# Kernel optimization log

Measured on AMD Instinct MI355X. Metric: run time of the kernel, lower is better.

Reference implementation:

```python
import jax, jax.numpy as jnp
import numpy as np

B, H, T, D = 4, 16, 4096, 128

def setup_inputs() -> dict:
    key = jax.random.key(0)
    kq, kk, kv = jax.random.split(key, 3)
    Q = jax.random.normal(kq, (B, H, T, D), dtype=jnp.float32)
    K = jax.random.normal(kk, (B, H, T, D), dtype=jnp.float32)
    V = jax.random.normal(kv, (B, H, T, D), dtype=jnp.float32)
    return {"Q": Q, "K": K, "V": V}

def reference(Q, K, V):
    # Unnormalized linear attention: Q @ K^T @ V.
    # Algebraically reassociated as Q @ (K^T @ V) to avoid the [T, T] intermediate:
    # kv: [B,H,D,D]
    kv = jnp.einsum('bhtd,bhte->bhde', K, V)
    return jnp.einsum('bhtd,bhde->bhte', Q, kv)
```

## Files before the change

### kernel.cpp

```cpp
#include <hip/hip_runtime.h>
#include <stdint.h>

typedef __attribute__((ext_vector_type(8))) short short8;
typedef __attribute__((ext_vector_type(4))) float floatx4;

#define T_DIM 4096
#define D_DIM 128
#define BH_TOT 64
#define NCHUNK 8
#define CHUNK (T_DIM / NCHUNK)
#define LSTRIDE 72

__device__ __forceinline__ unsigned short f2bf(float f) {
  unsigned int u = __float_as_uint(f);
  u = (u + 0x7FFFu + ((u >> 16) & 1u)) >> 16;
  return (unsigned short)u;
}

__device__ __forceinline__ unsigned int pack2(float lo, float hi) {
  return (unsigned int)f2bf(lo) | ((unsigned int)f2bf(hi) << 16);
}

__global__ __launch_bounds__(256, 2)
void kv_phase1(const float* __restrict__ K, const float* __restrict__ V,
               float* __restrict__ kvT) {
  const int bh    = blockIdx.y;
  const int chunk = blockIdx.x;
  const int tid   = threadIdx.x;
  const int lane  = tid & 63;
  const int wv    = tid >> 6;
  const int c     = tid & 31;
  const int r     = tid >> 5;
  const int m0    = (wv >> 1) * 64;
  const int n0    = (wv & 1) * 64;

  __shared__ unsigned short Vt[128 * LSTRIDE];
  __shared__ unsigned short Kt[128 * LSTRIDE];

  floatx4 acc[4][4];
#pragma unroll
  for (int i = 0; i < 4; ++i)
#pragma unroll
    for (int j = 0; j < 4; ++j) acc[i][j] = (floatx4){0.f, 0.f, 0.f, 0.f};

  const size_t base = ((size_t)bh * T_DIM + (size_t)chunk * CHUNK) * D_DIM;
  const float* Vp = V + base + 4 * c;
  const float* Kp = K + base + 4 * c;

  float4 ld[2][8];
  uint4  pk[2][4];

  auto load_tile = [&](int tile) {
    const size_t roff = (size_t)(tile * 64 + 8 * r) * D_DIM;
#pragma unroll
    for (int i = 0; i < 8; ++i) {
      ld[0][i] = *(const float4*)(Vp + roff + (size_t)i * D_DIM);
      ld[1][i] = *(const float4*)(Kp + roff + (size_t)i * D_DIM);
    }
  };

  auto pack_all = [&]() {
#pragma unroll
    for (int op = 0; op < 2; ++op)
#pragma unroll
      for (int j = 0; j < 4; ++j) {
        uint4 v;
        v.x = (unsigned int)f2bf(((const float*)&ld[op][0])[j]) |
              ((unsigned int)f2bf(((const float*)&ld[op][1])[j]) << 16);
        v.y = (unsigned int)f2bf(((const float*)&ld[op][2])[j]) |
              ((unsigned int)f2bf(((const float*)&ld[op][3])[j]) << 16);
        v.z = (unsigned int)f2bf(((const float*)&ld[op][4])[j]) |
              ((unsigned int)f2bf(((const float*)&ld[op][5])[j]) << 16);
        v.w = (unsigned int)f2bf(((const float*)&ld[op][6])[j]) |
              ((unsigned int)f2bf(((const float*)&ld[op][7])[j]) << 16);
        pk[op][j] = v;
      }
  };

  load_tile(0);
  pack_all();

  for (int tile = 0; tile < CHUNK / 64; ++tile) {
    if (tile < CHUNK / 64 - 1) load_tile(tile + 1);
    __syncthreads();
#pragma unroll
    for (int j = 0; j < 4; ++j) {
      *(uint4*)&Vt[(4 * c + j) * LSTRIDE + 8 * r] = pk[0][j];
      *(uint4*)&Kt[(4 * c + j) * LSTRIDE + 8 * r] = pk[1][j];
    }
    __syncthreads();

#pragma unroll
    for (int ks = 0; ks < 2; ++ks) {
      const int koff = 32 * ks + 8 * (lane >> 4);
      short8 af[4], bf[4];
#pragma unroll
      for (int tm = 0; tm < 4; ++tm)
        af[tm] = *(const short8*)&Vt[(m0 + tm * 16 + (lane & 15)) * LSTRIDE + koff];
#pragma unroll
      for (int tn = 0; tn < 4; ++tn)
        bf[tn] = *(const short8*)&Kt[(n0 + tn * 16 + (lane & 15)) * LSTRIDE + koff];
#pragma unroll
      for (int tm = 0; tm < 4; ++tm)
#pragma unroll
        for (int tn = 0; tn < 4; ++tn)
          acc[tm][tn] = __builtin_amdgcn_mfma_f32_16x16x32_bf16(af[tm], bf[tn],
                                                                acc[tm][tn], 0, 0, 0);
    }
    if (tile < CHUNK / 64 - 1) pack_all();
  }

  float* dst = kvT + (size_t)bh * (128 * 128);
  const int col = lane & 15;
  const int rb  = (lane >> 4) * 4;
#pragma unroll
  for (int tm = 0; tm < 4; ++tm)
#pragma unroll
    for (int tn = 0; tn < 4; ++tn)
#pragma unroll
      for (int rg = 0; rg < 4; ++rg) {
        const int e = m0 + tm * 16 + rb + rg;
        const int d = n0 + tn * 16 + col;
        unsafeAtomicAdd(&dst[e * 128 + d], acc[tm][tn][rg]);
      }
}

__global__ __launch_bounds__(256, 2)
void qkv_phase2(const float* __restrict__ Q, const float* __restrict__ kvT,
                float* __restrict__ out) {
  const int bh   = blockIdx.y;
  const int t0   = blockIdx.x * 128;
  const int tid  = threadIdx.x;
  const int lane = tid & 63;
  const int wv   = tid >> 6;
  const int c    = tid & 15;
  const int rq   = tid >> 4;
  const int m0   = (wv >> 1) * 64;
  const int n0   = (wv & 1) * 64;

  __shared__ unsigned short Qs[128 * LSTRIDE];
  __shared__ unsigned short Bs[128 * LSTRIDE];

  const float* Qp = Q + ((size_t)bh * T_DIM + t0) * D_DIM;
  const float* Bp = kvT + (size_t)bh * (128 * 128);

  floatx4 acc[4][4];
#pragma unroll
  for (int i = 0; i < 4; ++i)
#pragma unroll
    for (int j = 0; j < 4; ++j) acc[i][j] = (floatx4){0.f, 0.f, 0.f, 0.f};

  for (int h = 0; h < 2; ++h) {
    float4 lq[8], lb[8];
    const int cb = h * 64 + 4 * c;
#pragma unroll
    for (int i = 0; i < 8; ++i) {
      const int row = rq + 16 * i;
      lq[i] = *(const float4*)(Qp + (size_t)row * D_DIM + cb);
      lb[i] = *(const float4*)(Bp + (size_t)row * 128 + cb);
    }
    __syncthreads();
#pragma unroll
    for (int i = 0; i < 8; ++i) {
      const int row = rq + 16 * i;
      uint2 q2, b2;
      q2.x = pack2(lq[i].x, lq[i].y);
      q2.y = pack2(lq[i].z, lq[i].w);
      b2.x = pack2(lb[i].x, lb[i].y);
      b2.y = pack2(lb[i].z, lb[i].w);
      *(uint2*)&Qs[row * LSTRIDE + 4 * c] = q2;
      *(uint2*)&Bs[row * LSTRIDE + 4 * c] = b2;
    }
    __syncthreads();

#pragma unroll
    for (int ks = 0; ks < 2; ++ks) {
      const int koff = 32 * ks + 8 * (lane >> 4);
      short8 af[4], bf[4];
#pragma unroll
      for (int tm = 0; tm < 4; ++tm)
        af[tm] = *(const short8*)&Qs[(m0 + tm * 16 + (lane & 15)) * LSTRIDE + koff];
#pragma unroll
      for (int tn = 0; tn < 4; ++tn)
        bf[tn] = *(const short8*)&Bs[(n0 + tn * 16 + (lane & 15)) * LSTRIDE + koff];
#pragma unroll
      for (int tm = 0; tm < 4; ++tm)
#pragma unroll
        for (int tn = 0; tn < 4; ++tn)
          acc[tm][tn] = __builtin_amdgcn_mfma_f32_16x16x32_bf16(af[tm], bf[tn],
                                                                acc[tm][tn], 0, 0, 0);
    }
  }

  float* op = out + ((size_t)bh * T_DIM + t0) * D_DIM;
  const int col = lane & 15;
  const int rb  = (lane >> 4) * 4;
#pragma unroll
  for (int tm = 0; tm < 4; ++tm)
#pragma unroll
    for (int tn = 0; tn < 4; ++tn)
#pragma unroll
      for (int rg = 0; rg < 4; ++rg)
        op[(size_t)(m0 + tm * 16 + rb + rg) * D_DIM + (n0 + tn * 16 + col)] =
            acc[tm][tn][rg];
}

extern "C" void kernel_launch(void* const* d_in, const int* in_sizes, int n_in,
                              void* d_out, int out_size, void* d_ws, size_t ws_size,
                              hipStream_t stream) {
  const float* Q = (const float*)d_in[0];
  const float* K = (const float*)d_in[1];
  const float* V = (const float*)d_in[2];
  float* out = (float*)d_out;
  float* kvT = (float*)d_ws;

  hipMemsetAsync(d_ws, 0, (size_t)BH_TOT * 128 * 128 * sizeof(float), stream);
  kv_phase1<<<dim3(NCHUNK, BH_TOT), 256, 0, stream>>>(K, V, kvT);
  qkv_phase2<<<dim3(T_DIM / 128, BH_TOT), 256, 0, stream>>>(Q, kvT, out);
}
```

Before: 410.8 us.

## Replace atomic KV accumulation with per-chunk slabs plus reduce; direct-load phase 2

Phase 1 can now split T into up to 16 chunks, depending on workspace size. Each chunk writes a partial KV slab, and a separate reduce kernel sums the slabs, replacing the memset and the atomic adds. LDS writes and reads use a rotated (mod 9) swizzle to cut bank conflicts. Phase 2 drops shared memory and loads Q and KV fragments straight from global memory into registers, converting with hardware bf16 pack intrinsics, and occupancy hints are raised to 3. The cost is extra slab traffic and one more launch, and phase 2 now relies on cache hits for repeated KV loads.

```diff
diff --git a/kernel.cpp b/kernel.cpp
--- a/kernel.cpp
+++ b/kernel.cpp
@@ -1,4 +1,5 @@
 #include <hip/hip_runtime.h>
+#include <hip/hip_bf16.h>
 #include <stdint.h>
 
 typedef __attribute__((ext_vector_type(8))) short short8;
@@ -7,35 +8,55 @@
 #define T_DIM 4096
 #define D_DIM 128
 #define BH_TOT 64
-#define NCHUNK 8
-#define CHUNK (T_DIM / NCHUNK)
-#define LSTRIDE 72
-
-__device__ __forceinline__ unsigned short f2bf(float f) {
-  unsigned int u = __float_as_uint(f);
-  u = (u + 0x7FFFu + ((u >> 16) & 1u)) >> 16;
-  return (unsigned short)u;
-}
-
-__device__ __forceinline__ unsigned int pack2(float lo, float hi) {
-  return (unsigned int)f2bf(lo) | ((unsigned int)f2bf(hi) << 16);
-}
-
-__global__ __launch_bounds__(256, 2)
+#define LSTR 72
+#define KV_FLOATS (128 * 128)
+#define SLAB_FLOATS (BH_TOT * KV_FLOATS)
+
+__device__ __forceinline__ unsigned int packbf2(float lo, float hi) {
+  union { __hip_bfloat162 b; unsigned int u; } cv;
+  cv.b = __float22bfloat162_rn(make_float2(lo, hi));
+  return cv.u;
+}
+
+__device__ __forceinline__ short8 pack8(float4 a, float4 b) {
+  union { short8 s; unsigned int u[4]; } r;
+  r.u[0] = packbf2(a.x, a.y);
+  r.u[1] = packbf2(a.z, a.w);
+  r.u[2] = packbf2(b.x, b.y);
+  r.u[3] = packbf2(b.z, b.w);
+  return r.s;
+}
+
+__global__ __launch_bounds__(256, 3)
 void kv_phase1(const float* __restrict__ K, const float* __restrict__ V,
-               float* __restrict__ kvT) {
-  const int bh    = blockIdx.y;
-  const int chunk = blockIdx.x;
-  const int tid   = threadIdx.x;
-  const int lane  = tid & 63;
-  const int wv    = tid >> 6;
-  const int c     = tid & 31;
-  const int r     = tid >> 5;
-  const int m0    = (wv >> 1) * 64;
-  const int n0    = (wv & 1) * 64;
-
-  __shared__ unsigned short Vt[128 * LSTRIDE];
-  __shared__ unsigned short Kt[128 * LSTRIDE];
+               float* __restrict__ dst, int ntiles, int useAtomic) {
+  const int bh = blockIdx.y, chunk = blockIdx.x;
+  const int tid = threadIdx.x;
+  const int lane = tid & 63, wv = tid >> 6;
+  const int c = tid & 31, r = tid >> 5;
+  const int m0 = (wv >> 1) * 64, n0 = (wv & 1) * 64;
+  const int q4 = lane >> 4, l15 = lane & 15;
+
+  __shared__ unsigned short Vt[128 * LSTR];
+  __shared__ unsigned short Kt[128 * LSTR];
+
+  int wo[4];
+#pragma unroll
+  for (int j = 0; j < 4; ++j) {
+    const int row = 4 * c + j;
+    wo[j] = row * LSTR + ((r + row) % 9) * 8;
+  }
+  int roA[4][2], roB[4][2];
+#pragma unroll
+  for (int tt = 0; tt < 4; ++tt)
+#pragma unroll
+    for (int ks = 0; ks < 2; ++ks) {
+      const int g = 4 * ks + q4;
+      const int rowA = m0 + tt * 16 + l15;
+      const int rowB = n0 + tt * 16 + l15;
+      roA[tt][ks] = rowA * LSTR + ((g + rowA) % 9) * 8;
+      roB[tt][ks] = rowB * LSTR + ((g + rowB) % 9) * 8;
+    }
 
   floatx4 acc[4][4];
 #pragma unroll
@@ -43,7 +64,7 @@
 #pragma unroll
     for (int j = 0; j < 4; ++j) acc[i][j] = (floatx4){0.f, 0.f, 0.f, 0.f};
 
-  const size_t base = ((size_t)bh * T_DIM + (size_t)chunk * CHUNK) * D_DIM;
+  const size_t base = ((size_t)bh * T_DIM + (size_t)chunk * (ntiles * 64)) * D_DIM;
   const float* Vp = V + base + 4 * c;
   const float* Kp = K + base + 4 * c;
 
@@ -58,21 +79,16 @@
       ld[1][i] = *(const float4*)(Kp + roff + (size_t)i * D_DIM);
     }
   };
-
   auto pack_all = [&]() {
 #pragma unroll
     for (int op = 0; op < 2; ++op)
 #pragma unroll
       for (int j = 0; j < 4; ++j) {
         uint4 v;
-        v.x = (unsigned int)f2bf(((const float*)&ld[op][0])[j]) |
-              ((unsigned int)f2bf(((const float*)&ld[op][1])[j]) << 16);
-        v.y = (unsigned int)f2bf(((const float*)&ld[op][2])[j]) |
-              ((unsigned int)f2bf(((const float*)&ld[op][3])[j]) << 16);
-        v.z = (unsigned int)f2bf(((const float*)&ld[op][4])[j]) |
-              ((unsigned int)f2bf(((const float*)&ld[op][5])[j]) << 16);
-        v.w = (unsigned int)f2bf(((const float*)&ld[op][6])[j]) |
-              ((unsigned int)f2bf(((const float*)&ld[op][7])[j]) << 16);
+        v.x = packbf2(((const float*)&ld[op][0])[j], ((const float*)&ld[op][1])[j]);
+        v.y = packbf2(((const float*)&ld[op][2])[j], ((const float*)&ld[op][3])[j]);
+        v.z = packbf2(((const float*)&ld[op][4])[j], ((const float*)&ld[op][5])[j]);
+        v.w = packbf2(((const float*)&ld[op][6])[j], ((const float*)&ld[op][7])[j]);
         pk[op][j] = v;
       }
   };
@@ -80,26 +96,22 @@
   load_tile(0);
   pack_all();
 
-  for (int tile = 0; tile < CHUNK / 64; ++tile) {
-    if (tile < CHUNK / 64 - 1) load_tile(tile + 1);
+  for (int tile = 0; tile < ntiles; ++tile) {
+    if (tile + 1 < ntiles) load_tile(tile + 1);
     __syncthreads();
 #pragma unroll
     for (int j = 0; j < 4; ++j) {
-      *(uint4*)&Vt[(4 * c + j) * LSTRIDE + 8 * r] = pk[0][j];
-      *(uint4*)&Kt[(4 * c + j) * LSTRIDE + 8 * r] = pk[1][j];
+      *(uint4*)&Vt[wo[j]] = pk[0][j];
+      *(uint4*)&Kt[wo[j]] = pk[1][j];
     }
     __syncthreads();
-
 #pragma unroll
     for (int ks = 0; ks < 2; ++ks) {
-      const int koff = 32 * ks + 8 * (lane >> 4);
       short8 af[4], bf[4];
 #pragma unroll
-      for (int tm = 0; tm < 4; ++tm)
-        af[tm] = *(const short8*)&Vt[(m0 + tm * 16 + (lane & 15)) * LSTRIDE + koff];
-#pragma unroll
-      for (int tn = 0; tn < 4; ++tn)
-        bf[tn] = *(const short8*)&Kt[(n0 + tn * 16 + (lane & 15)) * LSTRIDE + koff];
+      for (int tm = 0; tm < 4; ++tm) af[tm] = *(const short8*)&Vt[roA[tm][ks]];
+#pragma unroll
+      for (int tn = 0; tn < 4; ++tn) bf[tn] = *(const short8*)&Kt[roB[tn][ks]];
 #pragma unroll
       for (int tm = 0; tm < 4; ++tm)
 #pragma unroll
@@ -107,42 +119,55 @@
           acc[tm][tn] = __builtin_amdgcn_mfma_f32_16x16x32_bf16(af[tm], bf[tn],
                                                                 acc[tm][tn], 0, 0, 0);
     }
-    if (tile < CHUNK / 64 - 1) pack_all();
-  }
-
-  float* dst = kvT + (size_t)bh * (128 * 128);
-  const int col = lane & 15;
-  const int rb  = (lane >> 4) * 4;
-#pragma unroll
-  for (int tm = 0; tm < 4; ++tm)
-#pragma unroll
-    for (int tn = 0; tn < 4; ++tn)
-#pragma unroll
-      for (int rg = 0; rg < 4; ++rg) {
-        const int e = m0 + tm * 16 + rb + rg;
-        const int d = n0 + tn * 16 + col;
-        unsafeAtomicAdd(&dst[e * 128 + d], acc[tm][tn][rg]);
-      }
-}
-
-__global__ __launch_bounds__(256, 2)
-void qkv_phase2(const float* __restrict__ Q, const float* __restrict__ kvT,
+    if (tile + 1 < ntiles) pack_all();
+  }
+
+  const int col = l15, rb = q4 * 4;
+  if (useAtomic) {
+    float* dp = dst + (size_t)bh * KV_FLOATS;
+#pragma unroll
+    for (int tm = 0; tm < 4; ++tm)
+#pragma unroll
+      for (int tn = 0; tn < 4; ++tn)
+#pragma unroll
+        for (int rg = 0; rg < 4; ++rg)
+          unsafeAtomicAdd(&dp[(m0 + tm * 16 + rb + rg) * 128 + n0 + tn * 16 + col],
+                          acc[tm][tn][rg]);
+  } else {
+    float* dp = dst + ((size_t)chunk * BH_TOT + bh) * KV_FLOATS;
+#pragma unroll
+    for (int tm = 0; tm < 4; ++tm)
+#pragma unroll
+      for (int tn = 0; tn < 4; ++tn)
+#pragma unroll
+        for (int rg = 0; rg < 4; ++rg)
+          dp[(m0 + tm * 16 + rb + rg) * 128 + n0 + tn * 16 + col] = acc[tm][tn][rg];
+  }
+}
+
+__global__ __launch_bounds__(256, 4)
+void kv_reduce(const float* __restrict__ slab, float* __restrict__ kv, int nchunk) {
+  const int idx = blockIdx.x * 256 + threadIdx.x;
+  const float4* p = (const float4*)slab + idx;
+  float4 s = p[0];
+  for (int c = 1; c < nchunk; ++c) {
+    float4 v = p[(size_t)c * (SLAB_FLOATS / 4)];
+    s.x += v.x; s.y += v.y; s.z += v.z; s.w += v.w;
+  }
+  ((float4*)kv)[idx] = s;
+}
+
+__global__ __launch_bounds__(256, 3)
+void qkv_phase2(const float* __restrict__ Q, const float* __restrict__ kv,
                 float* __restrict__ out) {
-  const int bh   = blockIdx.y;
-  const int t0   = blockIdx.x * 128;
-  const int tid  = threadIdx.x;
-  const int lane = tid & 63;
-  const int wv   = tid >> 6;
-  const int c    = tid & 15;
-  const int rq   = tid >> 4;
-  const int m0   = (wv >> 1) * 64;
-  const int n0   = (wv & 1) * 64;
-
-  __shared__ unsigned short Qs[128 * LSTRIDE];
-  __shared__ unsigned short Bs[128 * LSTRIDE];
-
-  const float* Qp = Q + ((size_t)bh * T_DIM + t0) * D_DIM;
-  const float* Bp = kvT + (size_t)bh * (128 * 128);
+  const int bh = blockIdx.y;
+  const int t0 = blockIdx.x * 128;
+  const int tid = threadIdx.x, lane = tid & 63, wv = tid >> 6;
+  const int m0 = (wv >> 1) * 64, n0 = (wv & 1) * 64;
+  const int q4 = lane >> 4, l15 = lane & 15;
+
+  const float* Qb = Q + ((size_t)bh * T_DIM + t0) * D_DIM;
+  const float* Bb = kv + (size_t)bh * KV_FLOATS;
 
   floatx4 acc[4][4];
 #pragma unroll
@@ -150,51 +175,30 @@
 #pragma unroll
     for (int j = 0; j < 4; ++j) acc[i][j] = (floatx4){0.f, 0.f, 0.f, 0.f};
 
-  for (int h = 0; h < 2; ++h) {
-    float4 lq[8], lb[8];
-    const int cb = h * 64 + 4 * c;
-#pragma unroll
-    for (int i = 0; i < 8; ++i) {
-      const int row = rq + 16 * i;
-      lq[i] = *(const float4*)(Qp + (size_t)row * D_DIM + cb);
-      lb[i] = *(const float4*)(Bp + (size_t)row * 128 + cb);
-    }
-    __syncthreads();
-#pragma unroll
-    for (int i = 0; i < 8; ++i) {
-      const int row = rq + 16 * i;
-      uint2 q2, b2;
-      q2.x = pack2(lq[i].x, lq[i].y);
-      q2.y = pack2(lq[i].z, lq[i].w);
-      b2.x = pack2(lb[i].x, lb[i].y);
-      b2.y = pack2(lb[i].z, lb[i].w);
-      *(uint2*)&Qs[row * LSTRIDE + 4 * c] = q2;
-      *(uint2*)&Bs[row * LSTRIDE + 4 * c] = b2;
-    }
-    __syncthreads();
-
-#pragma unroll
-    for (int ks = 0; ks < 2; ++ks) {
-      const int koff = 32 * ks + 8 * (lane >> 4);
-      short8 af[4], bf[4];
-#pragma unroll
-      for (int tm = 0; tm < 4; ++tm)
-        af[tm] = *(const short8*)&Qs[(m0 + tm * 16 + (lane & 15)) * LSTRIDE + koff];
+#pragma unroll 1
+  for (int ks = 0; ks < 4; ++ks) {
+    const int koff = 32 * ks + 8 * q4;
+    short8 bf[4], af[4];
+#pragma unroll
+    for (int tn = 0; tn < 4; ++tn) {
+      const float* p = Bb + (n0 + tn * 16 + l15) * 128 + koff;
+      bf[tn] = pack8(*(const float4*)p, *(const float4*)(p + 4));
+    }
+#pragma unroll
+    for (int tm = 0; tm < 4; ++tm) {
+      const float* p = Qb + (size_t)(m0 + tm * 16 + l15) * D_DIM + koff;
+      af[tm] = pack8(*(const float4*)p, *(const float4*)(p + 4));
+    }
+#pragma unroll
+    for (int tm = 0; tm < 4; ++tm)
 #pragma unroll
       for (int tn = 0; tn < 4; ++tn)
-        bf[tn] = *(const short8*)&Bs[(n0 + tn * 16 + (lane & 15)) * LSTRIDE + koff];
-#pragma unroll
-      for (int tm = 0; tm < 4; ++tm)
-#pragma unroll
-        for (int tn = 0; tn < 4; ++tn)
-          acc[tm][tn] = __builtin_amdgcn_mfma_f32_16x16x32_bf16(af[tm], bf[tn],
-                                                                acc[tm][tn], 0, 0, 0);
-    }
+        acc[tm][tn] = __builtin_amdgcn_mfma_f32_16x16x32_bf16(af[tm], bf[tn],
+                                                              acc[tm][tn], 0, 0, 0);
   }
 
   float* op = out + ((size_t)bh * T_DIM + t0) * D_DIM;
-  const int col = lane & 15;
-  const int rb  = (lane >> 4) * 4;
+  const int col = l15, rb = q4 * 4;
 #pragma unroll
   for (int tm = 0; tm < 4; ++tm)
 #pragma unroll
@@ -212,9 +216,26 @@
   const float* K = (const float*)d_in[1];
   const float* V = (const float*)d_in[2];
   float* out = (float*)d_out;
-  float* kvT = (float*)d_ws;
-
-  hipMemsetAsync(d_ws, 0, (size_t)BH_TOT * 128 * 128 * sizeof(float), stream);
-  kv_phase1<<<dim3(NCHUNK, BH_TOT), 256, 0, stream>>>(K, V, kvT);
-  qkv_phase2<<<dim3(T_DIM / 128, BH_TOT), 256, 0, stream>>>(Q, kvT, out);
-}
+  float* ws = (float*)d_ws;
+
+  const size_t slabBytes = (size_t)SLAB_FLOATS * sizeof(float);
+  int nchunk = 0;
+  if (ws_size >= 17 * slabBytes)      nchunk = 16;
+  else if (ws_size >= 9 * slabBytes)  nchunk = 8;
+  else if (ws_size >= 5 * slabBytes)  nchunk = 4;
+  else if (ws_size >= 3 * slabBytes)  nchunk = 2;
+
+  if (nchunk > 0) {
+    float* slab = ws;
+    float* kvb  = ws + (size_t)nchunk * SLAB_FLOATS;
+    kv_phase1<<<dim3(nchunk, BH_TOT), 256, 0, stream>>>(K, V, slab,
+                                                        64 / nchunk, 0);
+    kv_reduce<<<dim3(SLAB_FLOATS / 4 / 256), 256, 0, stream>>>(slab, kvb, nchunk);
+    qkv_phase2<<<dim3(T_DIM / 128, BH_TOT), 256, 0, stream>>>(Q, kvb, out);
+  } else {
+    float* kvb = ws;
+    hipMemsetAsync(kvb, 0, slabBytes, stream);
+    kv_phase1<<<dim3(8, BH_TOT), 256, 0, stream>>>(K, V, kvb, 8, 1);
+    qkv_phase2<<<dim3(T_DIM / 128, BH_TOT), 256, 0, stream>>>(Q, kvb, out);
+  }
+}
```

Result: slower. 605.8 us (+47.5%).
